# Optimization experiments

Measured on AMD Instinct MI355X. Metric: run time of the kernel, lower is better.

Reference implementation:

```python
import math
import jax, jax.numpy as jnp
import numpy as np

TOPK = 2
CAPACITY_FACTOR = 1.25
MIN_CAPACITY = 4


def setup_inputs() -> dict:
    key = jax.random.key(0)
    k1, k2, k3, k4, k5 = jax.random.split(key, 5)
    B, T, H, W, D = 2, 8, 16, 16, 2048
    E, I = 16, 2048
    s = 1.0 / math.sqrt(D)
    return {
        "hidden_states": jax.random.normal(k1, (B, T, H, W, D), dtype=jnp.float32),
        "wg_weight": jax.random.normal(k2, (E, D), dtype=jnp.float32) * s,
        "gate_proj": jax.random.normal(k3, (E, I, D), dtype=jnp.float32) * s,
        "up_proj": jax.random.normal(k4, (E, I, D), dtype=jnp.float32) * s,
        "down_proj": jax.random.normal(k5, (E, D, I), dtype=jnp.float32) * (1.0 / math.sqrt(I)),
    }


def _moe_forward(x, wg, gp, up, dp):
    B, T, H, W, D = x.shape
    S = T * H * W
    # core_shape=(1,1,1): indexing tokens == calculate tokens, flatten (T,H,W)
    tokens = x.reshape(B, S, D).transpose(1, 0, 2).reshape(-1, D)  # (N, D)
    N = tokens.shape[0]
    E = wg.shape[0]

    logits = tokens.astype(jnp.float32) @ wg.T              # (N, E)
    gates = jax.nn.softmax(logits, axis=1)                  # (N, E)

    # static expert capacity: topk * max(ceil(N/E * cf), min_capacity)
    cap = TOPK * max(math.ceil(N / E * CAPACITY_FACTOR), MIN_CAPACITY)

    _, expert_index = jax.lax.top_k(gates, TOPK)            # (N, k)
    expert_mask = jax.nn.one_hot(expert_index, E, dtype=jnp.int32)  # (N, k, E)

    # aux load-balance loss (computed for fidelity)
    mask_aux = expert_mask.max(axis=1).astype(jnp.float32)  # (N, E)
    l_aux = (E ** 2) * jnp.mean(jnp.mean(mask_aux, axis=0) * jnp.mean(gates, axis=0))

    # normalize top-k probabilities (norm_topk_prob=True, topk>1)
    gates_s = jnp.clip(jnp.einsum('nke,ne->n', expert_mask.astype(gates.dtype), gates),
                       jnp.finfo(gates.dtype).eps)
    router_probs = gates / gates_s[:, None]                 # (N, E)

    # token priority: cumsum over (topk*N) flattened in topk-major order
    em = expert_mask.transpose(1, 0, 2).reshape(TOPK * N, E)  # (kN, E)
    tp = jnp.cumsum(em, axis=0) * em - 1
    tp = tp.reshape(TOPK, N, E).transpose(1, 0, 2).max(axis=1)  # (N, E)
    valid = (tp >= 0) & (tp < cap)
    tp = jnp.where(valid, tp, 0)
    dispatch_mask = (tp[:, :, None] == jnp.arange(cap)[None, None, :]) & valid[:, :, None]  # (N,E,C) bool
    combine_weights = router_probs[:, :, None] * dispatch_mask  # (N, E, C)

    # dispatch -> expert FFN (SwiGLU) -> combine
    dm = dispatch_mask.astype(tokens.dtype)
    dispatched = jnp.einsum('nec,nd->ecd', dm, tokens)      # (E, C, D)
    gate_out = jax.nn.silu(jnp.einsum('ecd,eid->eci', dispatched, gp))
    up_out = jnp.einsum('ecd,eid->eci', dispatched, up)
    expert_out = jnp.einsum('eci,edi->ecd', gate_out * up_out, dp)  # (E, C, D)
    combined = jnp.einsum('nec,ecd->nd', combine_weights, expert_out)  # (N, D)

    y = combined.reshape(S, B, D).transpose(1, 0, 2).reshape(B, T, H, W, D)
    return y, l_aux


def reference(hidden_states, wg_weight, gate_proj, up_proj, down_proj):
    y, _l_aux = _moe_forward(hidden_states, wg_weight, gate_proj, up_proj, down_proj)
    return y
```

## Files before the change

kernel.cpp:

```cpp
#include <hip/hip_runtime.h>
#include <hip/hip_bf16.h>
#include <cstdint>
#include <cstddef>

#define NTOK 4096
#define NEXP 16
#define DIM  2048
#define IDIM 2048
#define CAP  640
#define SEQ  2048

typedef float v4f __attribute__((ext_vector_type(4)));
typedef short v8s __attribute__((ext_vector_type(8)));
typedef unsigned int v4u __attribute__((ext_vector_type(4)));

__device__ __forceinline__ unsigned short f2b(float x) {
    union { float f; unsigned u; } c; c.f = x;
    unsigned r = c.u + 0x7FFFu + ((c.u >> 16) & 1u);
    return (unsigned short)(r >> 16);
}
__device__ __forceinline__ float b2f(unsigned short x) {
    union { unsigned u; float f; } c; c.u = ((unsigned)x) << 16;
    return c.f;
}
__device__ __forceinline__ unsigned cvt2(float a, float b) {
    unsigned r;
    asm("v_cvt_pk_bf16_f32 %0, %1, %2" : "=v"(r) : "v"(a), "v"(b));
    return r;
}

__device__ __forceinline__ void async16(const void* g, void* l) {
    __builtin_amdgcn_global_load_lds(
        (const __attribute__((address_space(1))) unsigned int*)g,
        (__attribute__((address_space(3))) unsigned int*)l,
        16, 0, 0);
}

__global__ __launch_bounds__(256) void router_kernel(
    const float* __restrict__ hidden, const float* __restrict__ wg,
    int* __restrict__ top1, int* __restrict__ top2,
    float* __restrict__ w1, float* __restrict__ w2)
{
    int wid  = threadIdx.x >> 6;
    int lane = threadIdx.x & 63;
    int n = blockIdx.x * 4 + wid;
    int e = lane & 15;
    int chunk = lane >> 4;
    const float* tok  = hidden + ((size_t)(n & 1) * SEQ + (n >> 1)) * DIM;
    const float* wrow = wg + (size_t)e * DIM;
    float acc = 0.f;
    int d0 = chunk * (DIM / 4);
    #pragma unroll 4
    for (int d = d0; d < d0 + DIM / 4; d += 4) {
        float4 t4 = *(const float4*)(tok + d);
        float4 g4 = *(const float4*)(wrow + d);
        acc += t4.x * g4.x + t4.y * g4.y + t4.z * g4.z + t4.w * g4.w;
    }
    acc += __shfl_down(acc, 32);
    acc += __shfl_down(acc, 16);
    float v = acc;
    float v1 = v; int i1 = e;
    #pragma unroll
    for (int off = 8; off; off >>= 1) {
        float ov = __shfl_xor(v1, off);
        int   oi = __shfl_xor(i1, off);
        if (ov > v1 || (ov == v1 && oi < i1)) { v1 = ov; i1 = oi; }
    }
    float v2 = (e == i1) ? -INFINITY : v; int i2 = e;
    #pragma unroll
    for (int off = 8; off; off >>= 1) {
        float ov = __shfl_xor(v2, off);
        int   oi = __shfl_xor(i2, off);
        if (ov > v2 || (ov == v2 && oi < i2)) { v2 = ov; i2 = oi; }
    }
    if (lane == 0) {
        float e2v = expf(v2 - v1);
        float inv = 1.f / (1.f + e2v);
        top1[n] = i1; top2[n] = i2;
        w1[n] = inv;  w2[n] = e2v * inv;
    }
}

__global__ __launch_bounds__(1024) void slot_kernel(
    const int* __restrict__ top1, const int* __restrict__ top2,
    int* __restrict__ slot1, int* __restrict__ slot2,
    int* __restrict__ exp_tok, int* __restrict__ counts)
{
    int w = threadIdx.x >> 6;
    int lane = threadIdx.x & 63;
    unsigned long long below = (lane == 0) ? 0ull : ((~0ull) >> (64 - lane));
    int base = 0;
    for (int c = 0; c < NTOK / 64; ++c) {
        int n = c * 64 + lane;
        bool p = (top1[n] == w);
        unsigned long long m = __ballot(p);
        if (p) {
            int s = base + __popcll(m & below);
            slot1[n] = s;
            if (s < CAP) exp_tok[w * CAP + s] = n;
        }
        base += __popcll(m);
    }
    for (int c = 0; c < NTOK / 64; ++c) {
        int n = c * 64 + lane;
        bool p = (top2[n] == w);
        unsigned long long m = __ballot(p);
        if (p) {
            int s = base + __popcll(m & below);
            slot2[n] = s;
            if (s < CAP) exp_tok[w * CAP + s] = n;
        }
        base += __popcll(m);
    }
    if (lane == 0) counts[w] = base < CAP ? base : CAP;
}

__global__ __launch_bounds__(256) void dispatch_kernel(
    const float* __restrict__ hidden, const int* __restrict__ exp_tok,
    const int* __restrict__ counts, unsigned short* __restrict__ disp)
{
    int s = blockIdx.x, e = blockIdx.y;
    unsigned short* dst = disp + ((size_t)e * CAP + s) * DIM + threadIdx.x * 8;
    if (s < counts[e]) {
        int n = exp_tok[e * CAP + s];
        const float* src = hidden + ((size_t)(n & 1) * SEQ + (n >> 1)) * DIM + threadIdx.x * 8;
        float4 a = *(const float4*)src;
        float4 b = *(const float4*)(src + 4);
        v4u o;
        o[0] = cvt2(a.x, a.y); o[1] = cvt2(a.z, a.w);
        o[2] = cvt2(b.x, b.y); o[3] = cvt2(b.z, b.w);
        *(v4u*)dst = o;
    } else {
        v8s z = {0, 0, 0, 0, 0, 0, 0, 0};
        *(v8s*)dst = z;
    }
}

#define BK 64

template<int NW, int ROUNDS>
__device__ __forceinline__ void stage_a(
    const unsigned short* __restrict__ gbase, int grow0, int k0, int rs,
    unsigned short* lds, int wv, int ln)
{
    int sr = ln >> 3;
    int cb = ln & 7;
    #pragma unroll
    for (int p = 0; p < ROUNDS; ++p) {
        int r = p * (NW * 8) + wv * 8 + sr;
        const unsigned short* g = gbase + (size_t)(grow0 + r) * rs + k0 + ((cb ^ (r & 7)) << 3);
        async16(g, lds + (p * (NW * 8) + wv * 8) * 64);
    }
}

template<int NT, int ROUNDS>
__device__ __forceinline__ void issue_bx(
    const float* __restrict__ gbase, int grow0, int k0, int rs,
    float4* regs, int tid)
{
    int cb = tid & 7;
    int r0 = tid >> 3;
    #pragma unroll
    for (int p = 0; p < ROUNDS; ++p) {
        const float* g = gbase + (size_t)(grow0 + p * (NT / 8) + r0) * rs + k0 + (cb << 3);
        regs[2 * p]     = *(const float4*)g;
        regs[2 * p + 1] = *(const float4*)(g + 4);
    }
}

template<int NT, int ROUNDS>
__device__ __forceinline__ void write_bx(
    const float4* regs, unsigned short* lds, int tid)
{
    int cb = tid & 7;
    int r0 = tid >> 3;
    #pragma unroll
    for (int p = 0; p < ROUNDS; ++p) {
        int r = p * (NT / 8) + r0;
        float4 x = regs[2 * p], y = regs[2 * p + 1];
        v4u o;
        o[0] = cvt2(x.x, x.y); o[1] = cvt2(x.z, x.w);
        o[2] = cvt2(y.x, y.y); o[3] = cvt2(y.z, y.w);
        *(v4u*)&lds[r * 64 + ((cb ^ (r & 7)) << 3)] = o;
    }
}

__device__ __forceinline__ void grid_decomp3(int bid, int& mi, int& ni, int& e) {
    int swz = (bid & 7) * 96 + (bid >> 3);
    mi = swz % 3;
    int t = swz / 3;
    ni = t & 15;
    e  = t >> 4;
}

__global__ __launch_bounds__(512, 2) void gateup_kernel(
    const unsigned short* __restrict__ disp, const float* __restrict__ gp,
    const float* __restrict__ up, const int* __restrict__ counts,
    unsigned short* __restrict__ hbuf)
{
    extern __shared__ unsigned short smem[];
    unsigned short* As  = smem;
    unsigned short* Bgs = smem + 16384;
    unsigned short* Bus = smem + 24576;
    int mi, ni, e;
    grid_decomp3(blockIdx.x, mi, ni, e);
    int m0 = mi * 256;
    if (m0 >= counts[e]) return;
    int n0 = ni * 128;
    int tid = threadIdx.x;
    int wv = tid >> 6, ln = tid & 63;
    int wm = wv >> 1, wn = wv & 1;
    int lrow = ln & 15, quad = ln >> 4;
    int sw = lrow & 7;

    const unsigned short* Ab = disp + (size_t)e * CAP * DIM;
    const float* Gb = gp + (size_t)e * IDIM * DIM;
    const float* Ub = up + (size_t)e * IDIM * DIM;

    int arow[4], brow[4];
    #pragma unroll
    for (int i = 0; i < 4; ++i) {
        arow[i] = (wm * 64 + i * 16 + lrow) * 64;
        brow[i] = (wn * 64 + i * 16 + lrow) * 64;
    }

    v4f accg[4][4], accu[4][4];
    #pragma unroll
    for (int i = 0; i < 4; ++i)
        #pragma unroll
        for (int j = 0; j < 4; ++j) { accg[i][j] = (v4f)0.f; accu[i][j] = (v4f)0.f; }

    float4 rg[4], ru[4];
    issue_bx<512, 2>(Gb, n0, 0, DIM, rg, tid);
    issue_bx<512, 2>(Ub, n0, 0, DIM, ru, tid);

    for (int k0 = 0; k0 < DIM; k0 += BK) {
        __syncthreads();
        stage_a<8, 4>(Ab, m0, k0, DIM, As, wv, ln);
        write_bx<512, 2>(rg, Bgs, tid);
        write_bx<512, 2>(ru, Bus, tid);
        __syncthreads();
        int kn = k0 + BK;
        if (kn < DIM) {
            issue_bx<512, 2>(Gb, n0, kn, DIM, rg, tid);
            issue_bx<512, 2>(Ub, n0, kn, DIM, ru, tid);
        }
        #pragma unroll
        for (int ks = 0; ks < BK; ks += 32) {
            int cq = ks >> 3;
            v8s a[4];
            #pragma unroll
            for (int i = 0; i < 4; ++i)
                a[i] = *(const v8s*)&As[arow[i] + (((cq + quad) ^ sw) << 3)];
            #pragma unroll
            for (int j = 0; j < 4; ++j) {
                v8s bg = *(const v8s*)&Bgs[brow[j] + (((cq + quad) ^ sw) << 3)];
                v8s bu = *(const v8s*)&Bus[brow[j] + (((cq + quad) ^ sw) << 3)];
                #pragma unroll
                for (int i = 0; i < 4; ++i) {
                    accg[i][j] = __builtin_amdgcn_mfma_f32_16x16x32_bf16(a[i], bg, accg[i][j], 0, 0, 0);
                    accu[i][j] = __builtin_amdgcn_mfma_f32_16x16x32_bf16(a[i], bu, accu[i][j], 0, 0, 0);
                }
            }
        }
    }
    unsigned short* hb = hbuf + (size_t)e * CAP * IDIM;
    #pragma unroll
    for (int i = 0; i < 4; ++i)
        #pragma unroll
        for (int j = 0; j < 4; ++j) {
            int row = m0 + wm * 64 + i * 16 + quad * 4;
            int col = n0 + wn * 64 + j * 16 + lrow;
            #pragma unroll
            for (int rg_ = 0; rg_ < 4; ++rg_) {
                if (row + rg_ < CAP) {
                    float g = accg[i][j][rg_], u = accu[i][j][rg_];
                    float hv = (g / (1.f + __expf(-g))) * u;
                    hb[(size_t)(row + rg_) * IDIM + col] = f2b(hv);
                }
            }
        }
}

__global__ __launch_bounds__(512, 2) void down_kernel(
    const unsigned short* __restrict__ hbuf, const float* __restrict__ dp,
    const int* __restrict__ counts, unsigned short* __restrict__ eo)
{
    extern __shared__ unsigned short smem[];
    unsigned short* As0 = smem;
    unsigned short* As1 = smem + 16384;
    unsigned short* Bs  = smem + 32768;
    int mi, ni, e;
    grid_decomp3(blockIdx.x, mi, ni, e);
    int m0 = mi * 256;
    if (m0 >= counts[e]) return;
    int n0 = ni * 128;
    int tid = threadIdx.x;
    int wv = tid >> 6, ln = tid & 63;
    int wm = wv >> 1, wn = wv & 1;
    int lrow = ln & 15, quad = ln >> 4;
    int sw = lrow & 7;

    const unsigned short* Ab = hbuf + (size_t)e * CAP * IDIM;
    const float* Db = dp + (size_t)e * DIM * IDIM;

    int arow[4], brow[4];
    #pragma unroll
    for (int i = 0; i < 4; ++i) {
        arow[i] = (wm * 64 + i * 16 + lrow) * 64;
        brow[i] = (wn * 64 + i * 16 + lrow) * 64;
    }

    v4f acc[4][4];
    #pragma unroll
    for (int i = 0; i < 4; ++i)
        #pragma unroll
        for (int j = 0; j < 4; ++j) acc[i][j] = (v4f)0.f;

    float4 rb[4];
    stage_a<8, 4>(Ab, m0, 0, IDIM, As0, wv, ln);
    issue_bx<512, 2>(Db, n0, 0, IDIM, rb, tid);

    for (int k0 = 0; k0 < IDIM; k0 += BK) {
        int cur = (k0 >> 6) & 1;
        unsigned short* Ac = cur ? As1 : As0;
        unsigned short* An = cur ? As0 : As1;
        __syncthreads();
        write_bx<512, 2>(rb, Bs, tid);
        __syncthreads();
        int kn = k0 + BK;
        if (kn < IDIM) {
            stage_a<8, 4>(Ab, m0, kn, IDIM, An, wv, ln);
            issue_bx<512, 2>(Db, n0, kn, IDIM, rb, tid);
        }
        #pragma unroll
        for (int ks = 0; ks < BK; ks += 32) {
            int cq = ks >> 3;
            v8s a[4];
            #pragma unroll
            for (int i = 0; i < 4; ++i)
                a[i] = *(const v8s*)&Ac[arow[i] + (((cq + quad) ^ sw) << 3)];
            #pragma unroll
            for (int j = 0; j < 4; ++j) {
                v8s b = *(const v8s*)&Bs[brow[j] + (((cq + quad) ^ sw) << 3)];
                #pragma unroll
                for (int i = 0; i < 4; ++i)
                    acc[i][j] = __builtin_amdgcn_mfma_f32_16x16x32_bf16(a[i], b, acc[i][j], 0, 0, 0);
            }
        }
    }
    unsigned short* ob = eo + (size_t)e * CAP * DIM;
    #pragma unroll
    for (int i = 0; i < 4; ++i)
        #pragma unroll
        for (int j = 0; j < 4; ++j) {
            int row = m0 + wm * 64 + i * 16 + quad * 4;
            int col = n0 + wn * 64 + j * 16 + lrow;
            #pragma unroll
            for (int rg_ = 0; rg_ < 4; ++rg_) {
                if (row + rg_ < CAP)
                    ob[(size_t)(row + rg_) * DIM + col] = f2b(acc[i][j][rg_]);
            }
        }
}

__global__ __launch_bounds__(256) void combine_kernel(
    const unsigned short* __restrict__ eo,
    const int* __restrict__ top1, const int* __restrict__ top2,
    const int* __restrict__ slot1, const int* __restrict__ slot2,
    const float* __restrict__ w1, const float* __restrict__ w2,
    float* __restrict__ out)
{
    int n = blockIdx.x;
    int d = threadIdx.x * 8;
    float acc[8];
    #pragma unroll
    for (int i = 0; i < 8; ++i) acc[i] = 0.f;
    int s1 = slot1[n], s2 = slot2[n];
    if (s1 < CAP) {
        const unsigned short* p = eo + ((size_t)top1[n] * CAP + s1) * DIM + d;
        float w = w1[n];
        v8s v = *(const v8s*)p;
        #pragma unroll
        for (int i = 0; i < 8; ++i) acc[i] += w * b2f((unsigned short)v[i]);
    }
    if (s2 < CAP) {
        const unsigned short* p = eo + ((size_t)top2[n] * CAP + s2) * DIM + d;
        float w = w2[n];
        v8s v = *(const v8s*)p;
        #pragma unroll
        for (int i = 0; i < 8; ++i) acc[i] += w * b2f((unsigned short)v[i]);
    }
    float* o = out + ((size_t)(n & 1) * SEQ + (n >> 1)) * DIM + d;
    float4 o0 = {acc[0], acc[1], acc[2], acc[3]};
    float4 o1 = {acc[4], acc[5], acc[6], acc[7]};
    *(float4*)o = o0;
    *(float4*)(o + 4) = o1;
}

extern "C" void kernel_launch(void* const* d_in, const int* in_sizes, int n_in,
                              void* d_out, int out_size, void* d_ws, size_t ws_size,
                              hipStream_t stream) {
    const float* hidden = (const float*)d_in[0];
    const float* wg     = (const float*)d_in[1];
    const float* gp     = (const float*)d_in[2];
    const float* up     = (const float*)d_in[3];
    const float* dp     = (const float*)d_in[4];
    float* out = (float*)d_out;
    char* ws = (char*)d_ws;

    int*   top1    = (int*)(ws + 0);
    int*   top2    = (int*)(ws + 16384);
    float* w1      = (float*)(ws + 32768);
    float* w2      = (float*)(ws + 49152);
    int*   slot1   = (int*)(ws + 65536);
    int*   slot2   = (int*)(ws + 81920);
    int*   counts  = (int*)(ws + 98304);
    int*   exp_tok = (int*)(ws + 98560);
    unsigned short* disp = (unsigned short*)(ws + 262144);
    unsigned short* hbuf = (unsigned short*)(ws + 262144 + 41943040ull);
    unsigned short* eo   = (unsigned short*)(ws + 262144 + 2ull*41943040ull);

    static bool attr_set = false;
    if (!attr_set) {
        hipFuncSetAttribute((const void*)gateup_kernel,
                            hipFuncAttributeMaxDynamicSharedMemorySize, 65536);
        hipFuncSetAttribute((const void*)down_kernel,
                            hipFuncAttributeMaxDynamicSharedMemorySize, 81920);
        attr_set = true;
    }

    const int NB = 3 * 16 * NEXP;

    router_kernel<<<NTOK / 4, 256, 0, stream>>>(hidden, wg, top1, top2, w1, w2);
    slot_kernel<<<1, 1024, 0, stream>>>(top1, top2, slot1, slot2, exp_tok, counts);
    dispatch_kernel<<<dim3(CAP, NEXP), 256, 0, stream>>>(hidden, exp_tok, counts, disp);
    gateup_kernel<<<NB, 512, 65536, stream>>>(disp, gp, up, counts, hbuf);
    down_kernel<<<NB, 512, 81920, stream>>>(hbuf, dp, counts, eo);
    combine_kernel<<<NTOK, 256, 0, stream>>>(eo, top1, top2, slot1, slot2, w1, w2, out);
}
```

Before: 1.074 ms.

## Double-buffer LDS in gate/up GEMM with ping-pong phased MFMA schedule

Reworks the gate/up expert GEMM main loop to double-buffer the A, gate-B and up-B tiles in LDS. It splits each K step into four MFMA phases, interleaving the next tile's async A loads, B register-to-LDS writes and global prefetches between barrier-separated compute blocks. It also raises MFMA wave priority during compute. The aim is to overlap memory traffic with matrix math and drop the two full syncthreads per K step. Dynamic LDS doubles to 128 KB per block, so likely only one block fits per CU instead of two, and the extra barriers and wrap-around prefetches add overhead.

```diff
diff --git a/kernel.cpp b/kernel.cpp
--- a/kernel.cpp
+++ b/kernel.cpp
@@ -34,6 +34,12 @@
         (const __attribute__((address_space(1))) unsigned int*)g,
         (__attribute__((address_space(3))) unsigned int*)l,
         16, 0, 0);
+}
+
+__device__ __forceinline__ void bar_raw() {
+    __builtin_amdgcn_sched_barrier(0);
+    __builtin_amdgcn_s_barrier();
+    __builtin_amdgcn_sched_barrier(0);
 }
 
 __global__ __launch_bounds__(256) void router_kernel(
@@ -138,6 +144,16 @@
 
 #define BK 64
 
+__device__ __forceinline__ void stage_a_part(
+    const unsigned short* __restrict__ gbase, int grow0, int k0, int rs,
+    unsigned short* lds, int wv, int ln, int p)
+{
+    int sr = ln >> 3;
+    int cb = ln & 7;
+    int r = p * 64 + wv * 8 + sr;
+    const unsigned short* g = gbase + (size_t)(grow0 + r) * rs + k0 + ((cb ^ (r & 7)) << 3);
+    async16(g, lds + (p * 64 + wv * 8) * 64);
+}
 template<int NW, int ROUNDS>
 __device__ __forceinline__ void stage_a(
     const unsigned short* __restrict__ gbase, int grow0, int k0, int rs,
@@ -199,9 +215,12 @@
     unsigned short* __restrict__ hbuf)
 {
     extern __shared__ unsigned short smem[];
-    unsigned short* As  = smem;
-    unsigned short* Bgs = smem + 16384;
-    unsigned short* Bus = smem + 24576;
+    unsigned short* As0 = smem;
+    unsigned short* As1 = smem + 16384;
+    unsigned short* Bg0 = smem + 32768;
+    unsigned short* Bg1 = smem + 40960;
+    unsigned short* Bu0 = smem + 49152;
+    unsigned short* Bu1 = smem + 57344;
     int mi, ni, e;
     grid_decomp3(blockIdx.x, mi, ni, e);
     int m0 = mi * 256;
@@ -231,38 +250,106 @@
         for (int j = 0; j < 4; ++j) { accg[i][j] = (v4f)0.f; accu[i][j] = (v4f)0.f; }
 
     float4 rg[4], ru[4];
+    stage_a<8, 4>(Ab, m0, 0, DIM, As0, wv, ln);
     issue_bx<512, 2>(Gb, n0, 0, DIM, rg, tid);
     issue_bx<512, 2>(Ub, n0, 0, DIM, ru, tid);
-
-    for (int k0 = 0; k0 < DIM; k0 += BK) {
-        __syncthreads();
-        stage_a<8, 4>(Ab, m0, k0, DIM, As, wv, ln);
-        write_bx<512, 2>(rg, Bgs, tid);
-        write_bx<512, 2>(ru, Bus, tid);
-        __syncthreads();
-        int kn = k0 + BK;
-        if (kn < DIM) {
-            issue_bx<512, 2>(Gb, n0, kn, DIM, rg, tid);
-            issue_bx<512, 2>(Ub, n0, kn, DIM, ru, tid);
-        }
-        #pragma unroll
-        for (int ks = 0; ks < BK; ks += 32) {
-            int cq = ks >> 3;
-            v8s a[4];
-            #pragma unroll
-            for (int i = 0; i < 4; ++i)
-                a[i] = *(const v8s*)&As[arow[i] + (((cq + quad) ^ sw) << 3)];
-            #pragma unroll
-            for (int j = 0; j < 4; ++j) {
-                v8s bg = *(const v8s*)&Bgs[brow[j] + (((cq + quad) ^ sw) << 3)];
-                v8s bu = *(const v8s*)&Bus[brow[j] + (((cq + quad) ^ sw) << 3)];
+    write_bx<512, 2>(rg, Bg0, tid);
+    write_bx<512, 2>(ru, Bu0, tid);
+    issue_bx<512, 2>(Gb, n0, BK, DIM, rg, tid);
+    issue_bx<512, 2>(Ub, n0, BK, DIM, ru, tid);
+    asm volatile("s_waitcnt vmcnt(8)" ::: "memory");
+    __builtin_amdgcn_sched_barrier(0);
+    asm volatile("s_waitcnt lgkmcnt(0)" ::: "memory");
+    __builtin_amdgcn_sched_barrier(0);
+    __builtin_amdgcn_s_barrier();
+    __builtin_amdgcn_sched_barrier(0);
+
+    for (int kt = 0; kt < 32; ++kt) {
+        unsigned short* Ac  = (kt & 1) ? As1 : As0;
+        unsigned short* An  = (kt & 1) ? As0 : As1;
+        unsigned short* Bgc = (kt & 1) ? Bg1 : Bg0;
+        unsigned short* Bgn = (kt & 1) ? Bg0 : Bg1;
+        unsigned short* Buc = (kt & 1) ? Bu1 : Bu0;
+        unsigned short* Bun = (kt & 1) ? Bu0 : Bu1;
+        int k1 = ((kt + 1) & 31) * BK;
+        int k2 = ((kt + 2) & 31) * BK;
+        v8s afr[4][2], bfr[4][2];
+        write_bx<512, 2>(rg, Bgn, tid);
+        stage_a_part(Ab, m0, k1, DIM, An, wv, ln, 0);
+        stage_a_part(Ab, m0, k1, DIM, An, wv, ln, 1);
+        #pragma unroll
+        for (int ii = 0; ii < 2; ++ii)
+            #pragma unroll
+            for (int s = 0; s < 2; ++s)
+                afr[ii][s] = *(const v8s*)&Ac[arow[ii] + (((4 * s + quad) ^ sw) << 3)];
+        #pragma unroll
+        for (int j = 0; j < 4; ++j)
+            #pragma unroll
+            for (int s = 0; s < 2; ++s)
+                bfr[j][s] = *(const v8s*)&Bgc[brow[j] + (((4 * s + quad) ^ sw) << 3)];
+        bar_raw();
+        __builtin_amdgcn_s_setprio(1);
+        #pragma unroll
+        for (int j = 0; j < 4; ++j)
+            #pragma unroll
+            for (int s = 0; s < 2; ++s)
                 #pragma unroll
-                for (int i = 0; i < 4; ++i) {
-                    accg[i][j] = __builtin_amdgcn_mfma_f32_16x16x32_bf16(a[i], bg, accg[i][j], 0, 0, 0);
-                    accu[i][j] = __builtin_amdgcn_mfma_f32_16x16x32_bf16(a[i], bu, accu[i][j], 0, 0, 0);
-                }
-            }
-        }
+                for (int ii = 0; ii < 2; ++ii)
+                    accg[ii][j] = __builtin_amdgcn_mfma_f32_16x16x32_bf16(afr[ii][s], bfr[j][s], accg[ii][j], 0, 0, 0);
+        __builtin_amdgcn_s_setprio(0);
+        bar_raw();
+        write_bx<512, 2>(ru, Bun, tid);
+        stage_a_part(Ab, m0, k1, DIM, An, wv, ln, 2);
+        stage_a_part(Ab, m0, k1, DIM, An, wv, ln, 3);
+        #pragma unroll
+        for (int ii = 0; ii < 2; ++ii)
+            #pragma unroll
+            for (int s = 0; s < 2; ++s)
+                afr[2 + ii][s] = *(const v8s*)&Ac[arow[2 + ii] + (((4 * s + quad) ^ sw) << 3)];
+        bar_raw();
+        __builtin_amdgcn_s_setprio(1);
+        #pragma unroll
+        for (int j = 0; j < 4; ++j)
+            #pragma unroll
+            for (int s = 0; s < 2; ++s)
+                #pragma unroll
+                for (int ii = 0; ii < 2; ++ii)
+                    accg[2 + ii][j] = __builtin_amdgcn_mfma_f32_16x16x32_bf16(afr[2 + ii][s], bfr[j][s], accg[2 + ii][j], 0, 0, 0);
+        __builtin_amdgcn_s_setprio(0);
+        bar_raw();
+        issue_bx<512, 2>(Gb, n0, k2, DIM, rg, tid);
+        #pragma unroll
+        for (int j = 0; j < 4; ++j)
+            #pragma unroll
+            for (int s = 0; s < 2; ++s)
+                bfr[j][s] = *(const v8s*)&Buc[brow[j] + (((4 * s + quad) ^ sw) << 3)];
+        bar_raw();
+        __builtin_amdgcn_s_setprio(1);
+        #pragma unroll
+        for (int j = 0; j < 4; ++j)
+            #pragma unroll
+            for (int s = 0; s < 2; ++s)
+                #pragma unroll
+                for (int ii = 0; ii < 2; ++ii)
+                    accu[ii][j] = __builtin_amdgcn_mfma_f32_16x16x32_bf16(afr[ii][s], bfr[j][s], accu[ii][j], 0, 0, 0);
+        __builtin_amdgcn_s_setprio(0);
+        bar_raw();
+        issue_bx<512, 2>(Ub, n0, k2, DIM, ru, tid);
+        asm volatile("s_waitcnt vmcnt(8)" ::: "memory");
+        __builtin_amdgcn_sched_barrier(0);
+        asm volatile("s_waitcnt lgkmcnt(0)" ::: "memory");
+        __builtin_amdgcn_sched_barrier(0);
+        bar_raw();
+        __builtin_amdgcn_s_setprio(1);
+        #pragma unroll
+        for (int j = 0; j < 4; ++j)
+            #pragma unroll
+            for (int s = 0; s < 2; ++s)
+                #pragma unroll
+                for (int ii = 0; ii < 2; ++ii)
+                    accu[2 + ii][j] = __builtin_amdgcn_mfma_f32_16x16x32_bf16(afr[2 + ii][s], bfr[j][s], accu[2 + ii][j], 0, 0, 0);
+        __builtin_amdgcn_s_setprio(0);
+        bar_raw();
     }
     unsigned short* hb = hbuf + (size_t)e * CAP * IDIM;
     #pragma unroll
@@ -424,7 +511,7 @@
     static bool attr_set = false;
     if (!attr_set) {
         hipFuncSetAttribute((const void*)gateup_kernel,
-                            hipFuncAttributeMaxDynamicSharedMemorySize, 65536);
+                            hipFuncAttributeMaxDynamicSharedMemorySize, 131072);
         hipFuncSetAttribute((const void*)down_kernel,
                             hipFuncAttributeMaxDynamicSharedMemorySize, 81920);
         attr_set = true;
@@ -435,7 +522,7 @@
     router_kernel<<<NTOK / 4, 256, 0, stream>>>(hidden, wg, top1, top2, w1, w2);
     slot_kernel<<<1, 1024, 0, stream>>>(top1, top2, slot1, slot2, exp_tok, counts);
     dispatch_kernel<<<dim3(CAP, NEXP), 256, 0, stream>>>(hidden, exp_tok, counts, disp);
-    gateup_kernel<<<NB, 512, 65536, stream>>>(disp, gp, up, counts, hbuf);
+    gateup_kernel<<<NB, 512, 131072, stream>>>(disp, gp, up, counts, hbuf);
     down_kernel<<<NB, 512, 81920, stream>>>(hbuf, dp, counts, eo);
     combine_kernel<<<NTOK, 256, 0, stream>>>(eo, top1, top2, slot1, slot2, w1, w2, out);
 }
```

New measurement: 1.088 ms. About the same (+1.3%).
